# Optimization experiments

Measured on AMD Instinct MI355X. Metric: run time of the kernel, lower is better.

Reference implementation:

```python
import jax, jax.numpy as jnp
import numpy as np

N = 50000
E = 800000
IN_F = 128
HID_F = 128
OUT_F = 64


def setup_inputs() -> dict:
    key = jax.random.key(0)
    ks = jax.random.split(key, 12)
    x = jax.random.normal(ks[0], (N, IN_F), dtype=jnp.float32)
    row0 = jax.random.randint(ks[1], (E,), 0, N, dtype=jnp.int32)
    col0 = jax.random.randint(ks[2], (E,), 0, N, dtype=jnp.int32)
    val0 = jax.random.uniform(ks[3], (E,), dtype=jnp.float32)
    row1 = jax.random.randint(ks[4], (E,), 0, N, dtype=jnp.int32)
    col1 = jax.random.randint(ks[5], (E,), 0, N, dtype=jnp.int32)
    val1 = jax.random.uniform(ks[6], (E,), dtype=jnp.float32)
    # GraphConvolution params, uniform(-stdv, stdv) with stdv = 1/sqrt(out_features)
    s0 = 1.0 / np.sqrt(HID_F)
    W0 = jax.random.uniform(ks[7], (IN_F, HID_F), minval=-s0, maxval=s0, dtype=jnp.float32)
    b0 = jax.random.uniform(ks[8], (HID_F,), minval=-s0, maxval=s0, dtype=jnp.float32)
    s1 = 1.0 / np.sqrt(OUT_F)
    W1 = jax.random.uniform(ks[9], (HID_F, OUT_F), minval=-s1, maxval=s1, dtype=jnp.float32)
    b1 = jax.random.uniform(ks[10], (OUT_F,), minval=-s1, maxval=s1, dtype=jnp.float32)
    return {"x": x, "row0": row0, "col0": col0, "val0": val0,
            "row1": row1, "col1": col1, "val1": val1,
            "W0": W0, "b0": b0, "W1": W1, "b1": b1}


def _gcn_layer(x, W, b, row, col, val):
    # support = x @ W ; out = spmm(adj, support) + b
    support = x @ W                       # [N, F_out]
    msgs = val[:, None] * support[col]    # [E, F_out] gather along edges
    out = jax.ops.segment_sum(msgs, row, num_segments=N)
    return out + b


def reference(x, row0, col0, val0, row1, col1, val1, W0, b0, W1, b1):
    # Layer 0: GC -> relu (dropout is identity in eval mode)
    h = _gcn_layer(x, W0, b0, row0, col0, val0)
    h = jax.nn.relu(h)
    # Layer 1 (final): GC only
    out = _gcn_layer(h, W1, b1, row1, col1, val1)
    return out
```

## Files before the change

### kernel.cpp

```cpp
#include <hip/hip_runtime.h>
#include <hip/hip_fp16.h>

#define N_NODES 50000
#define IN_F    128
#define HID_F   128
#define OUT_F   64
#define E_EDGES 800000

#define RPB   16
#define NBUCK ((N_NODES + RPB - 1) / RPB)
#define BCAP  384
#define BIN_T   512
#define BIN_EPT 16
#define BIN_EPB (BIN_T * BIN_EPT)
#define BIN_NB  ((E_EDGES + BIN_EPB - 1) / BIN_EPB)
#define G0_NB   ((N_NODES + 127) / 128)

typedef _Float16 half8 __attribute__((ext_vector_type(8)));
typedef float    floatx4 __attribute__((ext_vector_type(4)));

__global__ __launch_bounds__(256) void prep_kernel(const float* __restrict__ W0,
                                                   const float* __restrict__ W1,
                                                   __half* __restrict__ wt0,
                                                   __half* __restrict__ wt1,
                                                   int* __restrict__ gfill) {
    int tid = blockIdx.x * 256 + threadIdx.x;
    if (tid < IN_F * HID_F) {
        int k = tid >> 7, n = tid & 127;
        wt0[n * IN_F + k] = __float2half(W0[tid]);
    }
    if (tid < HID_F * OUT_F) {
        int k = tid / OUT_F, n = tid % OUT_F;
        wt1[n * HID_F + k] = __float2half(W1[tid]);
    }
    if (tid < 2 * NBUCK) gfill[tid] = 0;
}

union BinLds {
    struct { int lhist[NBUCK]; int lbase[NBUCK]; } h;
    _Float16 ws[HID_F * (IN_F + 8)];
};

__global__ __launch_bounds__(BIN_T) void bin_gemm_kernel(
        const int* __restrict__ row0, const int* __restrict__ col0, const float* __restrict__ val0,
        const int* __restrict__ row1, const int* __restrict__ col1, const float* __restrict__ val1,
        int* __restrict__ gfill, int2* __restrict__ bcv0, int2* __restrict__ bcv1,
        const float* __restrict__ x, const __half* __restrict__ wt0,
        __half* __restrict__ sup0, int M) {
    __shared__ BinLds lds;
    const int tid = threadIdx.x;

    if (blockIdx.y < 2) {
        if (blockIdx.x >= BIN_NB) return;
        const int g = blockIdx.y;
        const int*   rowi = g ? row1 : row0;
        const int*   coli = g ? col1 : col0;
        const float* vali = g ? val1 : val0;
        int*  gf  = gfill + g * NBUCK;
        int2* bcv = g ? bcv1 : bcv0;

        for (int i = tid; i < NBUCK; i += BIN_T) lds.h.lhist[i] = 0;
        __syncthreads();

        int rnk[BIN_EPT], bkt[BIN_EPT], cl[BIN_EPT], rw[BIN_EPT];
        float vl[BIN_EPT];
        const int e0 = blockIdx.x * BIN_EPB;
#pragma unroll
        for (int i = 0; i < BIN_EPT; ++i) {
            const int e = e0 + i * BIN_T + tid;
            bkt[i] = -1;
            if (e < E_EDGES) {
                const int r = rowi[e];
                rw[i] = r; cl[i] = coli[e]; vl[i] = vali[e];
                bkt[i] = r >> 4;
                rnk[i] = atomicAdd(&lds.h.lhist[bkt[i]], 1);
            }
        }
        __syncthreads();
        for (int i = tid; i < NBUCK; i += BIN_T) {
            const int c = lds.h.lhist[i];
            lds.h.lbase[i] = c ? atomicAdd(&gf[i], c) : 0;
        }
        __syncthreads();
#pragma unroll
        for (int i = 0; i < BIN_EPT; ++i) {
            if (bkt[i] >= 0) {
                const int pos = lds.h.lbase[bkt[i]] + rnk[i];
                if (pos < BCAP)
                    bcv[(long)bkt[i] * BCAP + pos] =
                        make_int2(((rw[i] & (RPB - 1)) << 16) | cl[i], __float_as_int(vl[i]));
            }
        }
    } else {
        constexpr int KP = IN_F + 8;
        constexpr int NT = HID_F / 16;
        for (int c = tid; c < HID_F * (IN_F / 8); c += BIN_T) {
            const int n = c / (IN_F / 8), ko = (c % (IN_F / 8)) * 8;
            *(half8*)&lds.ws[n * KP + ko] = *(const half8*)(wt0 + n * IN_F + ko);
        }
        __syncthreads();

        const int wv = tid >> 6, lane = tid & 63;
        const int quad = lane >> 4, l16 = lane & 15;
        const int rowb = blockIdx.x * 128 + wv * 16;
        const int arow = rowb + l16;

        floatx4 acc[NT] = {};
#pragma unroll
        for (int ks = 0; ks < IN_F; ks += 32) {
            half8 af = {};
            if (arow < M) {
                const float4* p = (const float4*)(x + (long)arow * IN_F + ks + quad * 8);
                float4 u = p[0], w = p[1];
                af[0] = (_Float16)u.x; af[1] = (_Float16)u.y;
                af[2] = (_Float16)u.z; af[3] = (_Float16)u.w;
                af[4] = (_Float16)w.x; af[5] = (_Float16)w.y;
                af[6] = (_Float16)w.z; af[7] = (_Float16)w.w;
            }
#pragma unroll
            for (int t = 0; t < NT; ++t) {
                half8 bf = *(const half8*)&lds.ws[(t * 16 + l16) * KP + ks + quad * 8];
                acc[t] = __builtin_amdgcn_mfma_f32_16x16x32_f16(af, bf, acc[t], 0, 0, 0);
            }
        }
#pragma unroll
        for (int t = 0; t < NT; ++t) {
            const int col = t * 16 + l16;
#pragma unroll
            for (int i = 0; i < 4; ++i) {
                const int row = rowb + quad * 4 + i;
                if (row < M) sup0[(long)row * HID_F + col] = __float2half(acc[t][i]);
            }
        }
    }
}

__global__ __launch_bounds__(256) void agg_gemm_kernel(const int* __restrict__ gfill,
                                                       const int2* __restrict__ bcv,
                                                       const __half* __restrict__ sup,
                                                       const float* __restrict__ bias,
                                                       const __half* __restrict__ wt1,
                                                       __half* __restrict__ sup1) {
    constexpr int HP = HID_F + 8;
    __shared__ int2 sbuf[BCAP];
    __shared__ int  cur[RPB];
    __shared__ int  st[RPB + 1];
    __shared__ _Float16 ht[16 * HP];
    const int tid  = threadIdx.x;
    const int wv   = tid >> 6;
    const int lane = tid & 63;
    const int b    = blockIdx.x;
    const int cnt  = min(gfill[b], BCAP);
    const int2* eb = bcv + (long)b * BCAP;
    const int f0   = lane * 2;

    int2 ed[2]; int rnk[2];
    if (tid < RPB) cur[tid] = 0;
    __syncthreads();
#pragma unroll
    for (int k = 0; k < 2; ++k) {
        const int e = tid + k * 256;
        if (e < cnt) {
            ed[k] = eb[e];
            rnk[k] = atomicAdd(&cur[ed[k].x >> 16], 1);
        }
    }
    __syncthreads();
    if (tid == 0) {
        int s = 0;
#pragma unroll
        for (int i = 0; i < RPB; ++i) { st[i] = s; s += cur[i]; }
        st[RPB] = s;
    }
    __syncthreads();
#pragma unroll
    for (int k = 0; k < 2; ++k) {
        const int e = tid + k * 256;
        if (e < cnt) sbuf[st[ed[k].x >> 16] + rnk[k]] = ed[k];
    }
    __syncthreads();

#pragma unroll
    for (int i = 0; i < 4; ++i) {
        const int r  = wv * 4 + i;
        const int s0 = st[r], s1 = st[r + 1];
        float acc0 = bias[f0];
        float acc1 = bias[f0 + 1];
        for (int j = s0; j < s1; j += 8) {
            const int n = s1 - j;
            int   pr[8];
            float v[8];
#pragma unroll
            for (int q = 0; q < 8; ++q) {
                if (q < n) {
                    int2 e2 = sbuf[j + q];
                    pr[q] = e2.x & 0xFFFF;
                    v[q]  = __int_as_float(e2.y);
                } else { pr[q] = 0; v[q] = 0.f; }
            }
            __half2 s8[8];
#pragma unroll
            for (int q = 0; q < 8; ++q)
                s8[q] = *(const __half2*)(sup + (long)pr[q] * HID_F + f0);
#pragma unroll
            for (int q = 0; q < 8; ++q) {
                float2 g = __half22float2(s8[q]);
                acc0 += v[q] * g.x; acc1 += v[q] * g.y;
            }
        }
        acc0 = acc0 > 0.f ? acc0 : 0.f;
        acc1 = acc1 > 0.f ? acc1 : 0.f;
        *(__half2*)&ht[r * HP + f0] = __floats2half2_rn(acc0, acc1);
    }
    __syncthreads();

    const int quad = lane >> 4, l16 = lane & 15;
    floatx4 oacc = {};
#pragma unroll
    for (int ks = 0; ks < HID_F; ks += 32) {
        half8 af = *(const half8*)&ht[l16 * HP + ks + quad * 8];
        half8 bf = *(const half8*)(wt1 + (long)(wv * 16 + l16) * HID_F + ks + quad * 8);
        oacc = __builtin_amdgcn_mfma_f32_16x16x32_f16(af, bf, oacc, 0, 0, 0);
    }
    const int r0 = b * 16;
#pragma unroll
    for (int i = 0; i < 4; ++i) {
        const int row = r0 + quad * 4 + i;
        sup1[(long)row * OUT_F + wv * 16 + l16] = __float2half(oacc[i]);
    }
}

__global__ __launch_bounds__(256) void spmm_l1_kernel(const int* __restrict__ gfill,
                                                      const int2* __restrict__ bcv,
                                                      const __half* __restrict__ sup,
                                                      const float* __restrict__ bias,
                                                      float* __restrict__ out) {
    __shared__ int2 sbuf[BCAP];
    __shared__ int  cur[RPB];
    __shared__ int  st[RPB + 1];
    const int tid  = threadIdx.x;
    const int wv   = tid >> 6;
    const int lane = tid & 63;
    const int b    = blockIdx.x;
    const int cnt  = min(gfill[NBUCK + b], BCAP);
    const int2* eb = bcv + (long)b * BCAP;
    const int eh = lane >> 5;
    const int li = lane & 31;
    const int f0 = li * 2;

    int2 ed[2]; int rnk[2];
    if (tid < RPB) cur[tid] = 0;
    __syncthreads();
#pragma unroll
    for (int k = 0; k < 2; ++k) {
        const int e = tid + k * 256;
        if (e < cnt) {
            ed[k] = eb[e];
            rnk[k] = atomicAdd(&cur[ed[k].x >> 16], 1);
        }
    }
    __syncthreads();
    if (tid == 0) {
        int s = 0;
#pragma unroll
        for (int i = 0; i < RPB; ++i) { st[i] = s; s += cur[i]; }
        st[RPB] = s;
    }
    __syncthreads();
#pragma unroll
    for (int k = 0; k < 2; ++k) {
        const int e = tid + k * 256;
        if (e < cnt) sbuf[st[ed[k].x >> 16] + rnk[k]] = ed[k];
    }
    __syncthreads();

#pragma unroll
    for (int i = 0; i < 4; ++i) {
        const int r  = wv * 4 + i;
        const int s0 = st[r], s1 = st[r + 1];
        float acc0 = eh ? 0.f : bias[f0];
        float acc1 = eh ? 0.f : bias[f0 + 1];
        for (int j = s0; j < s1; j += 16) {
            int   pr[8];
            float v[8];
#pragma unroll
            for (int q = 0; q < 8; ++q) {
                const int idx = j + 2 * q + eh;
                if (idx < s1) {
                    int2 e2 = sbuf[idx];
                    pr[q] = e2.x & 0xFFFF;
                    v[q]  = __int_as_float(e2.y);
                } else { pr[q] = 0; v[q] = 0.f; }
            }
            __half2 s8[8];
#pragma unroll
            for (int q = 0; q < 8; ++q)
                s8[q] = *(const __half2*)(sup + (long)pr[q] * OUT_F + f0);
#pragma unroll
            for (int q = 0; q < 8; ++q) {
                float2 g = __half22float2(s8[q]);
                acc0 += v[q] * g.x; acc1 += v[q] * g.y;
            }
        }
        acc0 += __shfl_xor(acc0, 32, 64);
        acc1 += __shfl_xor(acc1, 32, 64);
        if (eh == 0) {
            const int row = b * 16 + r;
            *(float2*)(out + (long)row * OUT_F + f0) = make_float2(acc0, acc1);
        }
    }
}

extern "C" void kernel_launch(void* const* d_in, const int* in_sizes, int n_in,
                              void* d_out, int out_size, void* d_ws, size_t ws_size,
                              hipStream_t stream) {
    const float* x    = (const float*)d_in[0];
    const int*   row0 = (const int*)d_in[1];
    const int*   col0 = (const int*)d_in[2];
    const float* val0 = (const float*)d_in[3];
    const int*   row1 = (const int*)d_in[4];
    const int*   col1 = (const int*)d_in[5];
    const float* val1 = (const float*)d_in[6];
    const float* W0   = (const float*)d_in[7];
    const float* b0   = (const float*)d_in[8];
    const float* W1   = (const float*)d_in[9];
    const float* b1   = (const float*)d_in[10];
    float* out = (float*)d_out;

    __half* sup0 = (__half*)d_ws;
    __half* sup1 = sup0 + (long)N_NODES * HID_F;
    int2* bcv0   = (int2*)(sup1 + (long)N_NODES * OUT_F);
    int2* bcv1   = bcv0 + (long)NBUCK * BCAP;
    int*  gfill  = (int*)(bcv1 + (long)NBUCK * BCAP);
    __half* wt0  = (__half*)(gfill + 2 * NBUCK + 2);
    __half* wt1  = wt0 + IN_F * HID_F;

    prep_kernel<<<(IN_F * HID_F + 255) / 256, 256, 0, stream>>>(W0, W1, wt0, wt1, gfill);

    bin_gemm_kernel<<<dim3(G0_NB, 3), BIN_T, 0, stream>>>(
        row0, col0, val0, row1, col1, val1, gfill, bcv0, bcv1,
        x, wt0, sup0, N_NODES);

    agg_gemm_kernel<<<NBUCK, 256, 0, stream>>>(gfill, bcv0, sup0, b0, wt1, sup1);

    spmm_l1_kernel<<<NBUCK, 256, 0, stream>>>(gfill, bcv1, sup1, b1, out);
}
```

Measured before the change: 177.9 us.

## Move layer-1 edge binning into aggregation kernel and widen gather vectors

Layer-1 edge binning now runs as an extra grid slice of the layer-0 aggregation kernel instead of the first GEMM kernel, which rebalances work across the two launches. The separate lbase array is dropped, so the histogram array is reused in place for global offsets and LDS use shrinks. The aggregation loop now has each half-wave take alternate edges and gather 4 halfs per lane, with a cross-half shuffle reduction at the end, which doubles in-flight gathers per wave. The costs are extra shuffles and a larger LDS union in the aggregation kernel, which may lower occupancy there.

Result: slower. 187.5 us (+5.4%).

```diff
diff --git a/kernel.cpp b/kernel.cpp
--- a/kernel.cpp
+++ b/kernel.cpp
@@ -14,9 +14,14 @@
 #define BIN_EPT 16
 #define BIN_EPB (BIN_T * BIN_EPT)
 #define BIN_NB  ((E_EDGES + BIN_EPB - 1) / BIN_EPB)
+#define B1_EPT  8
+#define B1_EPB  (256 * B1_EPT)
+#define B1_NB   ((E_EDGES + B1_EPB - 1) / B1_EPB)
 #define G0_NB   ((N_NODES + 127) / 128)
+#define HP      (HID_F + 8)
 
 typedef _Float16 half8 __attribute__((ext_vector_type(8)));
+typedef _Float16 hv4   __attribute__((ext_vector_type(4)));
 typedef float    floatx4 __attribute__((ext_vector_type(4)));
 
 __global__ __launch_bounds__(256) void prep_kernel(const float* __restrict__ W0,
@@ -36,30 +41,22 @@
     if (tid < 2 * NBUCK) gfill[tid] = 0;
 }
 
-union BinLds {
-    struct { int lhist[NBUCK]; int lbase[NBUCK]; } h;
+union D1Lds {
+    int lhist[NBUCK];
     _Float16 ws[HID_F * (IN_F + 8)];
 };
 
-__global__ __launch_bounds__(BIN_T) void bin_gemm_kernel(
+__global__ __launch_bounds__(BIN_T) void bin0_gemm_kernel(
         const int* __restrict__ row0, const int* __restrict__ col0, const float* __restrict__ val0,
-        const int* __restrict__ row1, const int* __restrict__ col1, const float* __restrict__ val1,
-        int* __restrict__ gfill, int2* __restrict__ bcv0, int2* __restrict__ bcv1,
+        int* __restrict__ gfill, int2* __restrict__ bcv0,
         const float* __restrict__ x, const __half* __restrict__ wt0,
         __half* __restrict__ sup0, int M) {
-    __shared__ BinLds lds;
+    __shared__ D1Lds lds;
     const int tid = threadIdx.x;
 
-    if (blockIdx.y < 2) {
+    if (blockIdx.y == 0) {
         if (blockIdx.x >= BIN_NB) return;
-        const int g = blockIdx.y;
-        const int*   rowi = g ? row1 : row0;
-        const int*   coli = g ? col1 : col0;
-        const float* vali = g ? val1 : val0;
-        int*  gf  = gfill + g * NBUCK;
-        int2* bcv = g ? bcv1 : bcv0;
-
-        for (int i = tid; i < NBUCK; i += BIN_T) lds.h.lhist[i] = 0;
+        for (int i = tid; i < NBUCK; i += BIN_T) lds.lhist[i] = 0;
         __syncthreads();
 
         int rnk[BIN_EPT], bkt[BIN_EPT], cl[BIN_EPT], rw[BIN_EPT];
@@ -70,24 +67,24 @@
             const int e = e0 + i * BIN_T + tid;
             bkt[i] = -1;
             if (e < E_EDGES) {
-                const int r = rowi[e];
-                rw[i] = r; cl[i] = coli[e]; vl[i] = vali[e];
+                const int r = row0[e];
+                rw[i] = r; cl[i] = col0[e]; vl[i] = val0[e];
                 bkt[i] = r >> 4;
-                rnk[i] = atomicAdd(&lds.h.lhist[bkt[i]], 1);
+                rnk[i] = atomicAdd(&lds.lhist[bkt[i]], 1);
             }
         }
         __syncthreads();
         for (int i = tid; i < NBUCK; i += BIN_T) {
-            const int c = lds.h.lhist[i];
-            lds.h.lbase[i] = c ? atomicAdd(&gf[i], c) : 0;
+            const int c = lds.lhist[i];
+            lds.lhist[i] = c ? atomicAdd(&gfill[i], c) : 0;
         }
         __syncthreads();
 #pragma unroll
         for (int i = 0; i < BIN_EPT; ++i) {
             if (bkt[i] >= 0) {
-                const int pos = lds.h.lbase[bkt[i]] + rnk[i];
+                const int pos = lds.lhist[bkt[i]] + rnk[i];
                 if (pos < BCAP)
-                    bcv[(long)bkt[i] * BCAP + pos] =
+                    bcv0[(long)bkt[i] * BCAP + pos] =
                         make_int2(((rw[i] & (RPB - 1)) << 16) | cl[i], __float_as_int(vl[i]));
             }
         }
@@ -135,82 +132,141 @@
     }
 }
 
-__global__ __launch_bounds__(256) void agg_gemm_kernel(const int* __restrict__ gfill,
-                                                       const int2* __restrict__ bcv,
-                                                       const __half* __restrict__ sup,
-                                                       const float* __restrict__ bias,
-                                                       const __half* __restrict__ wt1,
-                                                       __half* __restrict__ sup1) {
-    constexpr int HP = HID_F + 8;
-    __shared__ int2 sbuf[BCAP];
-    __shared__ int  cur[RPB];
-    __shared__ int  st[RPB + 1];
-    __shared__ _Float16 ht[16 * HP];
-    const int tid  = threadIdx.x;
+union D2Lds {
+    int lhist[NBUCK];
+    struct {
+        int2 sbuf[BCAP];
+        int  cur[RPB];
+        int  st[RPB + 1];
+        _Float16 ht[16 * HP];
+    } a;
+};
+
+__global__ __launch_bounds__(256) void agg_bin1_kernel(
+        int* __restrict__ gfill, const int2* __restrict__ bcv0, int2* __restrict__ bcv1,
+        const int* __restrict__ row1, const int* __restrict__ col1, const float* __restrict__ val1,
+        const __half* __restrict__ sup, const float* __restrict__ bias,
+        const __half* __restrict__ wt1, __half* __restrict__ sup1) {
+    __shared__ D2Lds lds;
+    const int tid = threadIdx.x;
+
+    if (blockIdx.y == 1) {
+        if (blockIdx.x >= B1_NB) return;
+        int* gf = gfill + NBUCK;
+        for (int i = tid; i < NBUCK; i += 256) lds.lhist[i] = 0;
+        __syncthreads();
+
+        int rnk[B1_EPT], bkt[B1_EPT], cl[B1_EPT], rw[B1_EPT];
+        float vl[B1_EPT];
+        const int e0 = blockIdx.x * B1_EPB;
+#pragma unroll
+        for (int i = 0; i < B1_EPT; ++i) {
+            const int e = e0 + i * 256 + tid;
+            bkt[i] = -1;
+            if (e < E_EDGES) {
+                const int r = row1[e];
+                rw[i] = r; cl[i] = col1[e]; vl[i] = val1[e];
+                bkt[i] = r >> 4;
+                rnk[i] = atomicAdd(&lds.lhist[bkt[i]], 1);
+            }
+        }
+        __syncthreads();
+        for (int i = tid; i < NBUCK; i += 256) {
+            const int c = lds.lhist[i];
+            lds.lhist[i] = c ? atomicAdd(&gf[i], c) : 0;
+        }
+        __syncthreads();
+#pragma unroll
+        for (int i = 0; i < B1_EPT; ++i) {
+            if (bkt[i] >= 0) {
+                const int pos = lds.lhist[bkt[i]] + rnk[i];
+                if (pos < BCAP)
+                    bcv1[(long)bkt[i] * BCAP + pos] =
+                        make_int2(((rw[i] & (RPB - 1)) << 16) | cl[i], __float_as_int(vl[i]));
+            }
+        }
+        return;
+    }
+
     const int wv   = tid >> 6;
     const int lane = tid & 63;
+    const int eh   = lane >> 5;
+    const int li   = lane & 31;
     const int b    = blockIdx.x;
     const int cnt  = min(gfill[b], BCAP);
-    const int2* eb = bcv + (long)b * BCAP;
-    const int f0   = lane * 2;
-
-    int2 ed[2]; int rnk[2];
-    if (tid < RPB) cur[tid] = 0;
+    const int2* eb = bcv0 + (long)b * BCAP;
+
+    int2 ed[2]; int rnk2[2];
+    if (tid < RPB) lds.a.cur[tid] = 0;
     __syncthreads();
 #pragma unroll
     for (int k = 0; k < 2; ++k) {
         const int e = tid + k * 256;
         if (e < cnt) {
             ed[k] = eb[e];
-            rnk[k] = atomicAdd(&cur[ed[k].x >> 16], 1);
+            rnk2[k] = atomicAdd(&lds.a.cur[ed[k].x >> 16], 1);
         }
     }
     __syncthreads();
     if (tid == 0) {
         int s = 0;
 #pragma unroll
-        for (int i = 0; i < RPB; ++i) { st[i] = s; s += cur[i]; }
-        st[RPB] = s;
+        for (int i = 0; i < RPB; ++i) { lds.a.st[i] = s; s += lds.a.cur[i]; }
+        lds.a.st[RPB] = s;
     }
     __syncthreads();
 #pragma unroll
     for (int k = 0; k < 2; ++k) {
         const int e = tid + k * 256;
-        if (e < cnt) sbuf[st[ed[k].x >> 16] + rnk[k]] = ed[k];
+        if (e < cnt) lds.a.sbuf[lds.a.st[ed[k].x >> 16] + rnk2[k]] = ed[k];
     }
     __syncthreads();
 
 #pragma unroll
     for (int i = 0; i < 4; ++i) {
         const int r  = wv * 4 + i;
-        const int s0 = st[r], s1 = st[r + 1];
-        float acc0 = bias[f0];
-        float acc1 = bias[f0 + 1];
-        for (int j = s0; j < s1; j += 8) {
-            const int n = s1 - j;
+        const int s0 = lds.a.st[r], s1 = lds.a.st[r + 1];
+        float a0, a1, a2, a3;
+        if (eh == 0) {
+            a0 = bias[li * 4];     a1 = bias[li * 4 + 1];
+            a2 = bias[li * 4 + 2]; a3 = bias[li * 4 + 3];
+        } else a0 = a1 = a2 = a3 = 0.f;
+        for (int j = s0; j < s1; j += 16) {
             int   pr[8];
             float v[8];
 #pragma unroll
             for (int q = 0; q < 8; ++q) {
-                if (q < n) {
-                    int2 e2 = sbuf[j + q];
+                const int idx = j + 2 * q + eh;
+                if (idx < s1) {
+                    int2 e2 = lds.a.sbuf[idx];
                     pr[q] = e2.x & 0xFFFF;
                     v[q]  = __int_as_float(e2.y);
                 } else { pr[q] = 0; v[q] = 0.f; }
             }
-            __half2 s8[8];
+            hv4 s8[8];
 #pragma unroll
             for (int q = 0; q < 8; ++q)
-                s8[q] = *(const __half2*)(sup + (long)pr[q] * HID_F + f0);
+                s8[q] = *(const hv4*)(sup + (long)pr[q] * HID_F + li * 4);
 #pragma unroll
             for (int q = 0; q < 8; ++q) {
-                float2 g = __half22float2(s8[q]);
-                acc0 += v[q] * g.x; acc1 += v[q] * g.y;
-            }
-        }
-        acc0 = acc0 > 0.f ? acc0 : 0.f;
-        acc1 = acc1 > 0.f ? acc1 : 0.f;
-        *(__half2*)&ht[r * HP + f0] = __floats2half2_rn(acc0, acc1);
+                a0 += v[q] * (float)s8[q][0];
+                a1 += v[q] * (float)s8[q][1];
+                a2 += v[q] * (float)s8[q][2];
+                a3 += v[q] * (float)s8[q][3];
+            }
+        }
+        a0 += __shfl_xor(a0, 32, 64);
+        a1 += __shfl_xor(a1, 32, 64);
+        a2 += __shfl_xor(a2, 32, 64);
+        a3 += __shfl_xor(a3, 32, 64);
+        if (eh == 0) {
+            hv4 h;
+            h[0] = (_Float16)(a0 > 0.f ? a0 : 0.f);
+            h[1] = (_Float16)(a1 > 0.f ? a1 : 0.f);
+            h[2] = (_Float16)(a2 > 0.f ? a2 : 0.f);
+            h[3] = (_Float16)(a3 > 0.f ? a3 : 0.f);
+            *(hv4*)&lds.a.ht[r * HP + li * 4] = h;
+        }
     }
     __syncthreads();
 
@@ -218,7 +274,7 @@
     floatx4 oacc = {};
 #pragma unroll
     for (int ks = 0; ks < HID_F; ks += 32) {
-        half8 af = *(const half8*)&ht[l16 * HP + ks + quad * 8];
+        half8 af = *(const half8*)&lds.a.ht[l16 * HP + ks + quad * 8];
         half8 bf = *(const half8*)(wt1 + (long)(wv * 16 + l16) * HID_F + ks + quad * 8);
         oacc = __builtin_amdgcn_mfma_f32_16x16x32_f16(af, bf, oacc, 0, 0, 0);
     }
@@ -337,11 +393,11 @@
 
     prep_kernel<<<(IN_F * HID_F + 255) / 256, 256, 0, stream>>>(W0, W1, wt0, wt1, gfill);
 
-    bin_gemm_kernel<<<dim3(G0_NB, 3), BIN_T, 0, stream>>>(
-        row0, col0, val0, row1, col1, val1, gfill, bcv0, bcv1,
-        x, wt0, sup0, N_NODES);
-
-    agg_gemm_kernel<<<NBUCK, 256, 0, stream>>>(gfill, bcv0, sup0, b0, wt1, sup1);
+    bin0_gemm_kernel<<<dim3(G0_NB, 2), BIN_T, 0, stream>>>(
+        row0, col0, val0, gfill, bcv0, x, wt0, sup0, N_NODES);
+
+    agg_bin1_kernel<<<dim3(NBUCK, 2), 256, 0, stream>>>(
+        gfill, bcv0, bcv1, row1, col1, val1, sup0, b0, wt1, sup1);
 
     spmm_l1_kernel<<<NBUCK, 256, 0, stream>>>(gfill, bcv1, sup1, b1, out);
 }
```
